# Kernel optimization log

Measured on AMD Instinct MI355X. Metric: run time of the kernel, lower is better.

Reference implementation:

```python
import jax, jax.numpy as jnp
import numpy as np


def _conv(x, w, stride=1, pad=0):
    return jax.lax.conv_general_dilated(
        x, w, window_strides=(stride, stride),
        padding=[(pad, pad), (pad, pad)],
        dimension_numbers=('NCHW', 'OIHW', 'NCHW'))


def _frozen_bn(x, gamma, beta, mean, var):
    # FrozenBatchNorm2d: scale = gamma * rsqrt(var); bias = beta - mean*scale
    scale = gamma * jax.lax.rsqrt(var)
    bias = beta - mean * scale
    return x * scale[None, :, None, None] + bias[None, :, None, None]


def setup_inputs() -> dict:
    key = jax.random.key(0)
    ks = jax.random.split(key, 16)
    N, Cin, H, W = 32, 1024, 28, 28
    Cb, Cout = 256, 1024
    x = jax.random.normal(ks[0], (N, Cin, H, W), dtype=jnp.float32)
    # conv weights, kaiming-uniform-ish scale
    w1 = jax.random.uniform(ks[1], (Cb, Cin, 1, 1), minval=-1, maxval=1) * (1.0 / np.sqrt(Cin))
    w2 = jax.random.uniform(ks[2], (Cb, Cb, 3, 3), minval=-1, maxval=1) * (1.0 / np.sqrt(Cb * 9))
    w3 = jax.random.uniform(ks[3], (Cout, Cb, 1, 1), minval=-1, maxval=1) * (1.0 / np.sqrt(Cb))
    def bn_params(k, n):
        k1, k2, k3, k4 = jax.random.split(k, 4)
        gamma = jax.random.uniform(k1, (n,), minval=0.5, maxval=1.5)
        beta = jax.random.normal(k2, (n,)) * 0.1
        mean = jax.random.normal(k3, (n,)) * 0.1
        var = jax.random.uniform(k4, (n,), minval=0.5, maxval=1.5)
        return gamma, beta, mean, var
    g1, b1, m1, v1 = bn_params(ks[4], Cb)
    g2, b2, m2, v2 = bn_params(ks[5], Cb)
    g3, b3, m3, v3 = bn_params(ks[6], Cout)
    return dict(x=x, w1=w1, w2=w2, w3=w3,
                g1=g1, b1=b1, m1=m1, v1=v1,
                g2=g2, b2=b2, m2=m2, v2=v2,
                g3=g3, b3=b3, m3=m3, v3=v3)


def reference(x, w1, w2, w3, g1, b1, m1, v1, g2, b2, m2, v2, g3, b3, m3, v3):
    identity = x
    out = _conv(x, w1, stride=1, pad=0)          # 1x1: Cin -> Cb
    out = jax.nn.relu(_frozen_bn(out, g1, b1, m1, v1))
    out = _conv(out, w2, stride=1, pad=1)        # 3x3: Cb -> Cb
    out = jax.nn.relu(_frozen_bn(out, g2, b2, m2, v2))
    out = _conv(out, w3, stride=1, pad=0)        # 1x1: Cb -> Cout
    out = _frozen_bn(out, g3, b3, m3, v3)
    # stride==1 and in_channels==out_channels -> downsample is None
    out = jax.nn.relu(out + identity)
    return out
```

## Files before the change

kernel.cpp:

```cpp
#include <hip/hip_runtime.h>


#define BK 64

typedef __attribute__((ext_vector_type(8))) short short8;
typedef __attribute__((ext_vector_type(4))) float f32x4;

__device__ inline unsigned short f2bf(float f) {
    unsigned int u = __float_as_uint(f);
    u += 0x7fff + ((u >> 16) & 1);
    return (unsigned short)(u >> 16);
}

__device__ inline void gload16(const unsigned short* g, unsigned short* l) {
    __builtin_amdgcn_global_load_lds(
        (const __attribute__((address_space(1))) unsigned int*)g,
        (__attribute__((address_space(3))) unsigned int*)l, 16, 0, 0);
}

__global__ __launch_bounds__(256) void prep_w(
    const float* __restrict__ w1, const float* __restrict__ w2, const float* __restrict__ w3,
    const float* g1, const float* b1, const float* m1, const float* v1,
    const float* g2, const float* b2, const float* m2, const float* v2,
    const float* g3, const float* b3, const float* m3, const float* v3,
    unsigned short* __restrict__ Wb1, unsigned short* __restrict__ Wt2,
    unsigned short* __restrict__ Wb3,
    float* __restrict__ bn1, float* __restrict__ bn2, float* __restrict__ bn3) {
    int i = blockIdx.x * 256 + threadIdx.x;
    if (i < 262144) Wb1[i] = f2bf(w1[i]);
    if (i < 589824) {
        int kw = i % 3, t1 = i / 3;
        int kh = t1 % 3, t2 = t1 / 3;
        int ci = t2 & 255, co = t2 >> 8;
        Wt2[(size_t)((kh * 3 + kw) * 256 + co) * 256 + ci] = f2bf(w2[i]);
    }
    if (i < 262144) Wb3[i] = f2bf(w3[i]);
    if (i < 256) { float s = g1[i] * rsqrtf(v1[i]); bn1[i] = s; bn1[256 + i] = b1[i] - m1[i] * s; }
    if (i < 256) { float s = g2[i] * rsqrtf(v2[i]); bn2[i] = s; bn2[256 + i] = b2[i] - m2[i] * s; }
    if (i < 1024) { float s = g3[i] * rsqrtf(v3[i]); bn3[i] = s; bn3[1024 + i] = b3[i] - m3[i] * s; }
}

__global__ __launch_bounds__(256) void border_zero(uint4* __restrict__ y1p) {
    int i = blockIdx.x * 256 + threadIdx.x;
    int ch8 = i & 31;
    int t = i >> 5;
    int cell = t % 116;
    int n = t / 116;
    int h, w;
    if (cell < 30)      { h = 0;          w = cell; }
    else if (cell < 60) { h = 29;         w = cell - 30; }
    else if (cell < 88) { h = cell - 59;  w = 0; }
    else                { h = cell - 87;  w = 29; }
    y1p[((size_t)n * 900 + h * 30 + w) * 32 + ch8] = make_uint4(0u, 0u, 0u, 0u);
}

template <int CX, int NTAPS, int LAYER, int NT, int BMT>
__device__ __forceinline__ void conv_body(
    const float* __restrict__ Xf,
    const unsigned short* __restrict__ Xg, const unsigned short* __restrict__ Wg,
    const float* __restrict__ bn, int nco,
    const float* __restrict__ residual,
    unsigned short* __restrict__ obf, float* __restrict__ ofp) {
    __shared__ __align__(16) char smem[LAYER == 3 ? 33792 : (BMT * 128 + NT * 128)];
    unsigned short* Xs = (unsigned short*)smem;
    unsigned short* Ws = (unsigned short*)(smem + BMT * 128);
    const int tid = threadIdx.x;
    const int wave = tid >> 6, lane = tid & 63;
    const int quad = lane >> 4, l15 = lane & 15;
    const int Pb = blockIdx.x * BMT;
    const int cb = blockIdx.y * NT;
    const int wco = (wave & 1) * 64;
    const int wpx = (wave >> 1) * (BMT / 2);
    const int NWJ = BMT / 32;

    const int WR = NT / 32;
    const int XR = BMT / 32;
    int rowtW[4], csoW[4];
    #pragma unroll
    for (int t = 0; t < WR; ++t) {
        int slot = t * 256 + tid;
        int row = slot >> 3;
        int c = slot & 7;
        rowtW[t] = row;
        csoW[t] = ((c ^ (row & 7)) * 8);
    }

    int rowt[4], cso[4];
    size_t xrow[4];
    if (LAYER != 1) {
        #pragma unroll
        for (int t = 0; t < XR; ++t) {
            int slot = t * 256 + tid;
            int row = slot >> 3;
            int c = slot & 7;
            rowt[t] = row;
            cso[t] = ((c ^ (row & 7)) * 8);
            if (LAYER == 2) {
                int P = Pb + row;
                int n = P / 784, rem = P - n * 784;
                int h = rem / 28, w = rem - h * 28;
                xrow[t] = (size_t)n * 900 + h * 30 + w;
            } else {
                xrow[t] = (size_t)(Pb + row);
            }
        }
    }

    const int cpl = (lane >> 2) + (wave & 1) * 16;
    size_t xbase[2];
    int plr[2];
    if (LAYER == 1) {
        #pragma unroll
        for (int r = 0; r < 2; ++r) {
            int quarter = (wave >> 1) + 2 * r;
            int pl = quarter * 16 + (lane & 3) * 4;
            int P = Pb + pl;
            int n = P / 784, p = P - n * 784;
            plr[r] = pl;
            xbase[r] = ((size_t)n * 1024 + 2 * cpl) * 784 + p;
        }
    }

    f32x4 acc[4][4];
    #pragma unroll
    for (int i = 0; i < 4; ++i)
        #pragma unroll
        for (int j = 0; j < NWJ; ++j)
            acc[i][j] = (f32x4){0.f, 0.f, 0.f, 0.f};

    for (int tap = 0; tap < NTAPS; ++tap) {
        const int tapofs = (NTAPS == 9) ? ((tap / 3) * 30 + (tap % 3)) : 0;
        const unsigned short* Wtap = Wg + (size_t)tap * 256 * CX;
        for (int k0 = 0; k0 < CX; k0 += BK) {
            __syncthreads();
            #pragma unroll
            for (int t = 0; t < WR; ++t) {
                unsigned short* wl = Ws + (size_t)(t * 256 + wave * 64) * 8;
                gload16(Wtap + (size_t)(cb + rowtW[t]) * CX + k0 + csoW[t], wl);
            }
            if (LAYER == 1) {
                #pragma unroll
                for (int r = 0; r < 2; ++r) {
                    const float* src = Xf + xbase[r] + (size_t)k0 * 784;
                    float4 a = *(const float4*)src;
                    float4 b = *(const float4*)(src + 784);
                    float av[4] = {a.x, a.y, a.z, a.w};
                    float bv[4] = {b.x, b.y, b.z, b.w};
                    #pragma unroll
                    for (int j = 0; j < 4; ++j) {
                        unsigned u = (unsigned)f2bf(av[j]) | ((unsigned)f2bf(bv[j]) << 16);
                        int row = plr[r] + j;
                        int dw = row * 32 + (((cpl >> 2) ^ (row & 7)) << 2) + (cpl & 3);
                        ((unsigned*)Xs)[dw] = u;
                    }
                }
            } else {
                #pragma unroll
                for (int t = 0; t < XR; ++t) {
                    unsigned short* xl = Xs + (size_t)(t * 256 + wave * 64) * 8;
                    gload16(Xg + (xrow[t] + tapofs) * (size_t)CX + k0 + cso[t], xl);
                }
            }
            __syncthreads();
            #pragma unroll
            for (int kk = 0; kk < BK; kk += 32) {
                short8 af[4], bf[4];
                const int cbase = kk >> 3;
                #pragma unroll
                for (int wi = 0; wi < 4; ++wi) {
                    int row = wco + wi * 16 + l15;
                    int ch = (cbase + quad) ^ (row & 7);
                    af[wi] = *(const short8*)(Ws + (row * 8 + ch) * 8);
                }
                #pragma unroll
                for (int wj = 0; wj < NWJ; ++wj) {
                    int row = wpx + wj * 16 + l15;
                    int ch = (cbase + quad) ^ (row & 7);
                    bf[wj] = *(const short8*)(Xs + (row * 8 + ch) * 8);
                }
                #pragma unroll
                for (int wi = 0; wi < 4; ++wi)
                    #pragma unroll
                    for (int wj = 0; wj < NWJ; ++wj)
                        acc[wi][wj] = __builtin_amdgcn_mfma_f32_16x16x32_bf16(
                            af[wi], bf[wj], acc[wi][wj], 0, 0, 0);
            }
        }
    }

    __syncthreads();

    if (LAYER == 3) {
        float* ep = (float*)smem;
        #pragma unroll
        for (int pass = 0; pass < 2; ++pass) {
            if ((wave & 1) == pass) {
                #pragma unroll
                for (int wi = 0; wi < 4; ++wi) {
                    int co0 = cb + wco + wi * 16 + quad * 4;
                    f32x4 sc = *(const f32x4*)(bn + co0);
                    f32x4 bi = *(const f32x4*)(bn + nco + co0);
                    int cr0 = wi * 16 + quad * 4;
                    #pragma unroll
                    for (int wj = 0; wj < 4; ++wj) {
                        int px = wpx + wj * 16 + l15;
                        #pragma unroll
                        for (int r = 0; r < 4; ++r)
                            ep[(cr0 + r) * 132 + px] = fmaf(acc[wi][wj][r], sc[r], bi[r]);
                    }
                }
            }
            __syncthreads();
            {
                int cr = tid >> 2;
                int cg = tid & 3;
                int co = cb + pass * 64 + cr;
                #pragma unroll
                for (int k = 0; k < 8; ++k) {
                    int px4 = (cg + 4 * k) * 4;
                    f32x4 v = *(const f32x4*)(ep + cr * 132 + px4);
                    int P = Pb + px4;
                    int n = P / 784, p = P - n * 784;
                    size_t off = ((size_t)n * 1024 + co) * 784 + p;
                    float4 rs = *(const float4*)(residual + off);
                    float4 o;
                    o.x = v[0] + rs.x; o.x = o.x > 0.f ? o.x : 0.f;
                    o.y = v[1] + rs.y; o.y = o.y > 0.f ? o.y : 0.f;
                    o.z = v[2] + rs.z; o.z = o.z > 0.f ? o.z : 0.f;
                    o.w = v[3] + rs.w; o.w = o.w > 0.f ? o.w : 0.f;
                    *(float4*)(ofp + off) = o;
                }
            }
            __syncthreads();
        }
    } else {
        const int EPW = NT + 8;
        unsigned short* ep = (unsigned short*)smem;
        #pragma unroll
        for (int wi = 0; wi < 4; ++wi) {
            int co0 = cb + wco + wi * 16 + quad * 4;
            f32x4 sc = *(const f32x4*)(bn + co0);
            f32x4 bi = *(const f32x4*)(bn + nco + co0);
            int col = wco + wi * 16 + quad * 4;
            #pragma unroll
            for (int wj = 0; wj < NWJ; ++wj) {
                int pxl = wpx + wj * 16 + l15;
                float v0 = fmaf(acc[wi][wj][0], sc[0], bi[0]); v0 = v0 > 0.f ? v0 : 0.f;
                float v1 = fmaf(acc[wi][wj][1], sc[1], bi[1]); v1 = v1 > 0.f ? v1 : 0.f;
                float v2 = fmaf(acc[wi][wj][2], sc[2], bi[2]); v2 = v2 > 0.f ? v2 : 0.f;
                float v3 = fmaf(acc[wi][wj][3], sc[3], bi[3]); v3 = v3 > 0.f ? v3 : 0.f;
                uint2 pk;
                pk.x = (unsigned)f2bf(v0) | ((unsigned)f2bf(v1) << 16);
                pk.y = (unsigned)f2bf(v2) | ((unsigned)f2bf(v3) << 16);
                *(uint2*)(ep + pxl * EPW + col) = pk;
            }
        }
        __syncthreads();
        {
            int pxl = tid >> 2;
            int cg = tid & 3;
            int P = Pb + pxl;
            size_t orow;
            if (LAYER == 1) {
                int n = P / 784, rem = P - n * 784;
                int h = rem / 28, w = rem - h * 28;
                orow = (size_t)n * 900 + (h + 1) * 30 + (w + 1);
            } else {
                orow = (size_t)P;
            }
            #pragma unroll
            for (int k = 0; k < NT / 32; ++k) {
                int cc = (cg + 4 * k) * 8;
                uint4 v = *(const uint4*)(ep + pxl * EPW + cc);
                *(uint4*)(obf + orow * 256 + cb + cc) = v;
            }
        }
    }
}

__global__ __launch_bounds__(256) void conv1_mfma(
    const float* __restrict__ Xf, const unsigned short* __restrict__ Wg,
    const float* __restrict__ bn, unsigned short* __restrict__ obf) {
    conv_body<1024, 1, 1, 128, 64>(Xf, nullptr, Wg, bn, 256, nullptr, obf, nullptr);
}
__global__ __launch_bounds__(256) void conv2_mfma(
    const unsigned short* __restrict__ Xg, const unsigned short* __restrict__ Wg,
    const float* __restrict__ bn, unsigned short* __restrict__ obf) {
    conv_body<256, 9, 2, 128, 64>(nullptr, Xg, Wg, bn, 256, nullptr, obf, nullptr);
}
__global__ __launch_bounds__(256) void conv3_mfma(
    const unsigned short* __restrict__ Xg, const unsigned short* __restrict__ Wg,
    const float* __restrict__ bn, const float* __restrict__ residual,
    float* __restrict__ ofp) {
    conv_body<256, 1, 3, 128, 128>(nullptr, Xg, Wg, bn, 1024, residual, nullptr, ofp);
}

extern "C" void kernel_launch(void* const* d_in, const int* in_sizes, int n_in,
                              void* d_out, int out_size, void* d_ws, size_t ws_size,
                              hipStream_t stream) {
    const float* x  = (const float*)d_in[0];
    const float* w1 = (const float*)d_in[1];
    const float* w2 = (const float*)d_in[2];
    const float* w3 = (const float*)d_in[3];
    const float* g1 = (const float*)d_in[4];  const float* b1 = (const float*)d_in[5];
    const float* m1 = (const float*)d_in[6];  const float* v1 = (const float*)d_in[7];
    const float* g2 = (const float*)d_in[8];  const float* b2 = (const float*)d_in[9];
    const float* m2 = (const float*)d_in[10]; const float* v2 = (const float*)d_in[11];
    const float* g3 = (const float*)d_in[12]; const float* b3 = (const float*)d_in[13];
    const float* m3 = (const float*)d_in[14]; const float* v3 = (const float*)d_in[15];
    float* out = (float*)d_out;

    char* ws = (char*)d_ws;
    unsigned short* y1p = (unsigned short*)(ws);
    unsigned short* y2  = (unsigned short*)(ws + 14745600);
    unsigned short* Wb1 = (unsigned short*)(ws + 27590656);
    unsigned short* Wt2 = (unsigned short*)(ws + 28114944);
    unsigned short* Wb3 = (unsigned short*)(ws + 29294592);
    float* bn1 = (float*)(ws + 29818880);
    float* bn2 = (float*)(ws + 29820928);
    float* bn3 = (float*)(ws + 29822976);

    prep_w<<<2304, 256, 0, stream>>>(w1, w2, w3,
                                     g1, b1, m1, v1, g2, b2, m2, v2, g3, b3, m3, v3,
                                     Wb1, Wt2, Wb3, bn1, bn2, bn3);
    border_zero<<<464, 256, 0, stream>>>((uint4*)y1p);

    conv1_mfma<<<dim3(392, 2), 256, 0, stream>>>(x, Wb1, bn1, y1p);
    conv2_mfma<<<dim3(392, 2), 256, 0, stream>>>(y1p, Wt2, bn2, y2);
    conv3_mfma<<<dim3(196, 8), 256, 0, stream>>>(y2, Wb3, bn3, x, out);
}
```

Measured before the change: 325.7 us.

## Double-buffer LDS tiles to overlap global loads with MFMA compute

Restructures the conv main loop into a flattened tap×k step loop with two LDS stage buffers. The next step's weight and activation tiles (and, for layer 1, the fp32 loads and bf16 conversion) are issued before computing the current tile, and each step ends with one barrier instead of two. The goal is to hide global-memory latency behind MFMA work. In exchange, LDS use per block doubles, which may lower occupancy, and the explicit waitcnt/barrier handling has to be correct.

```diff
diff --git a/kernel.cpp b/kernel.cpp
--- a/kernel.cpp
+++ b/kernel.cpp
@@ -61,9 +61,23 @@
     const float* __restrict__ bn, int nco,
     const float* __restrict__ residual,
     unsigned short* __restrict__ obf, float* __restrict__ ofp) {
-    __shared__ __align__(16) char smem[LAYER == 3 ? 33792 : (BMT * 128 + NT * 128)];
-    unsigned short* Xs = (unsigned short*)smem;
-    unsigned short* Ws = (unsigned short*)(smem + BMT * 128);
+    constexpr int KSTEPS = CX / BK;
+    constexpr int NSTEP = NTAPS * KSTEPS;
+    constexpr int XB = BMT * BK * 2;
+    constexpr int WB = NT * BK * 2;
+    constexpr int STAGEB = 2 * (XB + WB);
+    constexpr int EPIB = (LAYER == 3) ? 64 * 132 * 4 : 64 * (NT + 8) * 2;
+    constexpr int SMEMB = STAGEB > EPIB ? STAGEB : EPIB;
+    constexpr int NWJ = BMT / 32;
+    constexpr int WR = NT / 32;
+    constexpr int XR = BMT / 32;
+
+    __shared__ __align__(16) char smem[SMEMB];
+    unsigned short* const Xs0 = (unsigned short*)smem;
+    unsigned short* const Xs1 = (unsigned short*)(smem + XB);
+    unsigned short* const Ws0 = (unsigned short*)(smem + 2 * XB);
+    unsigned short* const Ws1 = (unsigned short*)(smem + 2 * XB + WB);
+
     const int tid = threadIdx.x;
     const int wave = tid >> 6, lane = tid & 63;
     const int quad = lane >> 4, l15 = lane & 15;
@@ -71,21 +85,17 @@
     const int cb = blockIdx.y * NT;
     const int wco = (wave & 1) * 64;
     const int wpx = (wave >> 1) * (BMT / 2);
-    const int NWJ = BMT / 32;
-
-    const int WR = NT / 32;
-    const int XR = BMT / 32;
-    int rowtW[4], csoW[4];
+
+    size_t wro[WR];
     #pragma unroll
     for (int t = 0; t < WR; ++t) {
         int slot = t * 256 + tid;
         int row = slot >> 3;
         int c = slot & 7;
-        rowtW[t] = row;
-        csoW[t] = ((c ^ (row & 7)) * 8);
-    }
-
-    int rowt[4], cso[4];
+        wro[t] = (size_t)(cb + row) * CX + ((c ^ (row & 7)) * 8);
+    }
+
+    int cso[4];
     size_t xrow[4];
     if (LAYER != 1) {
         #pragma unroll
@@ -93,7 +103,6 @@
             int slot = t * 256 + tid;
             int row = slot >> 3;
             int c = slot & 7;
-            rowt[t] = row;
             cso[t] = ((c ^ (row & 7)) * 8);
             if (LAYER == 2) {
                 int P = Pb + row;
@@ -121,71 +130,109 @@
         }
     }
 
-    f32x4 acc[4][4];
+    auto stageW = [&](int s, unsigned short* wsb) {
+        int tap = (NTAPS == 1) ? 0 : (s / KSTEPS);
+        int k0 = (s - tap * KSTEPS) * BK;
+        const unsigned short* Wtap = Wg + (size_t)tap * 256 * CX;
+        #pragma unroll
+        for (int t = 0; t < WR; ++t)
+            gload16(Wtap + wro[t] + k0, wsb + (t * 256 + wave * 64) * 8);
+    };
+    auto stageX = [&](int s, unsigned short* xsb) {
+        int tap = (NTAPS == 1) ? 0 : (s / KSTEPS);
+        int k0 = (s - tap * KSTEPS) * BK;
+        int tapofs = (NTAPS == 9) ? ((tap / 3) * 30 + (tap % 3)) : 0;
+        #pragma unroll
+        for (int t = 0; t < XR; ++t)
+            gload16(Xg + (xrow[t] + tapofs) * (size_t)CX + k0 + cso[t],
+                    xsb + (t * 256 + wave * 64) * 8);
+    };
+    float4 xa[2], xb[2];
+    auto loadX1 = [&](int s) {
+        size_t k0 = (size_t)s * BK;
+        #pragma unroll
+        for (int r = 0; r < 2; ++r) {
+            const float* src = Xf + xbase[r] + k0 * 784;
+            xa[r] = *(const float4*)src;
+            xb[r] = *(const float4*)(src + 784);
+        }
+    };
+    auto convW1 = [&](unsigned short* xsb) {
+        #pragma unroll
+        for (int r = 0; r < 2; ++r) {
+            float av[4] = {xa[r].x, xa[r].y, xa[r].z, xa[r].w};
+            float bv[4] = {xb[r].x, xb[r].y, xb[r].z, xb[r].w};
+            #pragma unroll
+            for (int j = 0; j < 4; ++j) {
+                unsigned u = (unsigned)f2bf(av[j]) | ((unsigned)f2bf(bv[j]) << 16);
+                int row = plr[r] + j;
+                int dw = row * 32 + (((cpl >> 2) ^ (row & 7)) << 2) + (cpl & 3);
+                ((unsigned*)xsb)[dw] = u;
+            }
+        }
+    };
+
+    f32x4 acc[4][NWJ];
     #pragma unroll
     for (int i = 0; i < 4; ++i)
         #pragma unroll
         for (int j = 0; j < NWJ; ++j)
             acc[i][j] = (f32x4){0.f, 0.f, 0.f, 0.f};
 
-    for (int tap = 0; tap < NTAPS; ++tap) {
-        const int tapofs = (NTAPS == 9) ? ((tap / 3) * 30 + (tap % 3)) : 0;
-        const unsigned short* Wtap = Wg + (size_t)tap * 256 * CX;
-        for (int k0 = 0; k0 < CX; k0 += BK) {
-            __syncthreads();
-            #pragma unroll
-            for (int t = 0; t < WR; ++t) {
-                unsigned short* wl = Ws + (size_t)(t * 256 + wave * 64) * 8;
-                gload16(Wtap + (size_t)(cb + rowtW[t]) * CX + k0 + csoW[t], wl);
-            }
-            if (LAYER == 1) {
+    auto compute = [&](const unsigned short* xsb, const unsigned short* wsb) {
+        #pragma unroll
+        for (int kk = 0; kk < BK; kk += 32) {
+            short8 af[4], bf[NWJ];
+            const int cbase = kk >> 3;
+            #pragma unroll
+            for (int wi = 0; wi < 4; ++wi) {
+                int row = wco + wi * 16 + l15;
+                int ch = (cbase + quad) ^ (row & 7);
+                af[wi] = *(const short8*)(wsb + (row * 8 + ch) * 8);
+            }
+            #pragma unroll
+            for (int wj = 0; wj < NWJ; ++wj) {
+                int row = wpx + wj * 16 + l15;
+                int ch = (cbase + quad) ^ (row & 7);
+                bf[wj] = *(const short8*)(xsb + (row * 8 + ch) * 8);
+            }
+            #pragma unroll
+            for (int wi = 0; wi < 4; ++wi)
                 #pragma unroll
-                for (int r = 0; r < 2; ++r) {
-                    const float* src = Xf + xbase[r] + (size_t)k0 * 784;
-                    float4 a = *(const float4*)src;
-                    float4 b = *(const float4*)(src + 784);
-                    float av[4] = {a.x, a.y, a.z, a.w};
-                    float bv[4] = {b.x, b.y, b.z, b.w};
-                    #pragma unroll
-                    for (int j = 0; j < 4; ++j) {
-                        unsigned u = (unsigned)f2bf(av[j]) | ((unsigned)f2bf(bv[j]) << 16);
-                        int row = plr[r] + j;
-                        int dw = row * 32 + (((cpl >> 2) ^ (row & 7)) << 2) + (cpl & 3);
-                        ((unsigned*)Xs)[dw] = u;
-                    }
-                }
-            } else {
-                #pragma unroll
-                for (int t = 0; t < XR; ++t) {
-                    unsigned short* xl = Xs + (size_t)(t * 256 + wave * 64) * 8;
-                    gload16(Xg + (xrow[t] + tapofs) * (size_t)CX + k0 + cso[t], xl);
-                }
-            }
-            __syncthreads();
-            #pragma unroll
-            for (int kk = 0; kk < BK; kk += 32) {
-                short8 af[4], bf[4];
-                const int cbase = kk >> 3;
-                #pragma unroll
-                for (int wi = 0; wi < 4; ++wi) {
-                    int row = wco + wi * 16 + l15;
-                    int ch = (cbase + quad) ^ (row & 7);
-                    af[wi] = *(const short8*)(Ws + (row * 8 + ch) * 8);
-                }
-                #pragma unroll
-                for (int wj = 0; wj < NWJ; ++wj) {
-                    int row = wpx + wj * 16 + l15;
-                    int ch = (cbase + quad) ^ (row & 7);
-                    bf[wj] = *(const short8*)(Xs + (row * 8 + ch) * 8);
-                }
-                #pragma unroll
-                for (int wi = 0; wi < 4; ++wi)
-                    #pragma unroll
-                    for (int wj = 0; wj < NWJ; ++wj)
-                        acc[wi][wj] = __builtin_amdgcn_mfma_f32_16x16x32_bf16(
-                            af[wi], bf[wj], acc[wi][wj], 0, 0, 0);
-            }
-        }
+                for (int wj = 0; wj < NWJ; ++wj)
+                    acc[wi][wj] = __builtin_amdgcn_mfma_f32_16x16x32_bf16(
+                        af[wi], bf[wj], acc[wi][wj], 0, 0, 0);
+        }
+    };
+
+    stageW(0, Ws0);
+    if (LAYER == 1) { loadX1(0); convW1(Xs0); }
+    else            stageX(0, Xs0);
+    asm volatile("s_waitcnt vmcnt(0)" ::: "memory");
+    asm volatile("s_waitcnt lgkmcnt(0)" ::: "memory");
+    __builtin_amdgcn_s_barrier();
+    __builtin_amdgcn_sched_barrier(0);
+
+    int cur = 0;
+    #pragma unroll 1
+    for (int s = 0; s < NSTEP; ++s) {
+        unsigned short* xc = cur ? Xs1 : Xs0;
+        unsigned short* wc = cur ? Ws1 : Ws0;
+        unsigned short* xn = cur ? Xs0 : Xs1;
+        unsigned short* wn = cur ? Ws0 : Ws1;
+        const bool pre = (s + 1 < NSTEP);
+        if (pre) {
+            if (LAYER == 1) loadX1(s + 1);
+            stageW(s + 1, wn);
+            if (LAYER != 1) stageX(s + 1, xn);
+        }
+        compute(xc, wc);
+        if (LAYER == 1 && pre) convW1(xn);
+        asm volatile("s_waitcnt vmcnt(0)" ::: "memory");
+        if (LAYER == 1) asm volatile("s_waitcnt lgkmcnt(0)" ::: "memory");
+        __builtin_amdgcn_s_barrier();
+        __builtin_amdgcn_sched_barrier(0);
+        cur ^= 1;
     }
 
     __syncthreads();
@@ -234,7 +281,7 @@
             __syncthreads();
         }
     } else {
-        const int EPW = NT + 8;
+        constexpr int EPW = NT + 8;
         unsigned short* ep = (unsigned short*)smem;
         #pragma unroll
         for (int wi = 0; wi < 4; ++wi) {
```

After: 322.2 us. Within noise of the previous version (-1.1%).
